# Kernel optimization log

Measured on AMD Instinct MI355X. Metric: run time of the kernel, lower is better.

Reference implementation:

```python
import jax, jax.numpy as jnp
import numpy as np

T, B, A = 64, 512, 5
XD, YD, ZD, HD, MD = 2, 10, 16, 200, 90
HMIC, HMAC = 200, 200


def setup_inputs() -> dict:
    key = jax.random.key(0)
    ks = jax.random.split(key, 40)
    it = iter(range(40))
    def nrm(shape, s=0.05):
        return jax.random.normal(ks[next(it)], shape, jnp.float32) * s
    inp = {}
    inp["y"] = jax.random.normal(ks[next(it)], (T, B, YD), jnp.float32)
    # values in {-1} u [0, MD): -1 means "sample macro goal"
    inp["macro_goals"] = jax.random.randint(ks[next(it)], (T, B, A), 0, MD + 1, jnp.int32) - 1
    # dec_macro: Linear(YD+HMAC,HD) ReLU Linear(HD,MD) LogSoftmax
    inp["Wdm1"] = nrm((A, YD + HMAC, HD)); inp["bdm1"] = nrm((A, HD))
    inp["Wdm2"] = nrm((A, HD, MD));        inp["bdm2"] = nrm((A, MD))
    # prior: Linear(MD+HMIC,HD) ReLU Linear(HD,HD) ReLU
    inp["Wpr1"] = nrm((A, MD + HMIC, HD)); inp["bpr1"] = nrm((A, HD))
    inp["Wpr2"] = nrm((A, HD, HD));        inp["bpr2"] = nrm((A, HD))
    inp["Wpm"] = nrm((A, HD, ZD)); inp["bpm"] = nrm((A, ZD))
    inp["Wps"] = nrm((A, HD, ZD)); inp["bps"] = nrm((A, ZD))
    # dec: Linear(YD+MD+ZD+HMIC,HD) ReLU Linear(HD,HD) ReLU
    inp["Wd1"] = nrm((A, YD + MD + ZD + HMIC, HD)); inp["bd1"] = nrm((A, HD))
    inp["Wd2"] = nrm((A, HD, HD));                  inp["bd2"] = nrm((A, HD))
    inp["Wdx"] = nrm((A, HD, XD)); inp["bdx"] = nrm((A, XD))
    inp["Wds"] = nrm((A, HD, XD)); inp["bds"] = nrm((A, XD))
    # per-agent micro GRU (input XD+ZD, hidden HMIC), torch gate order [r;z;n]
    inp["Wih_mic"] = nrm((A, 3 * HMIC, XD + ZD)); inp["Whh_mic"] = nrm((A, 3 * HMIC, HMIC))
    inp["bih_mic"] = nrm((A, 3 * HMIC));          inp["bhh_mic"] = nrm((A, 3 * HMIC))
    # macro GRU (input A*MD, hidden HMAC)
    inp["Wih_mac"] = nrm((3 * HMAC, A * MD)); inp["Whh_mac"] = nrm((3 * HMAC, HMAC))
    inp["bih_mac"] = nrm((3 * HMAC,));        inp["bhh_mac"] = nrm((3 * HMAC,))
    # pre-drawn sampling noise: gumbel for multinomial, standard normal for gaussians
    u = jax.random.uniform(ks[next(it)], (T - 1, A, B, MD), jnp.float32, 1e-6, 1.0 - 1e-6)
    inp["eps_g"] = -jnp.log(-jnp.log(u))
    inp["eps_z"] = jax.random.normal(ks[next(it)], (T - 1, A, B, ZD), jnp.float32)
    inp["eps_x"] = jax.random.normal(ks[next(it)], (T - 1, A, B, XD), jnp.float32)
    inp["burn_in"] = 8
    return inp


def reference(y, Wdm1, bdm1, Wdm2, bdm2, Wpr1, bpr1, Wpr2, bpr2, Wpm, bpm, Wps, bps,
              Wd1, bd1, Wd2, bd2, Wdx, bdx, Wds, bds,
              Wih_mic, Whh_mic, bih_mic, bhh_mic, Wih_mac, Whh_mac, bih_mac, bhh_mac,
              eps_g, eps_z, eps_x, macro_goals, burn_in):
    def lin(x, W, b):  # per-agent linear: x [A,B,I], W [A,I,O]
        return jnp.einsum('abi,aio->abo', x, W) + b[:, None]

    def gru1(x, h, Wih, Whh, bih, bhh):  # x [B,I], h [B,H]
        gi = x @ Wih.T + bih
        gh = h @ Whh.T + bhh
        ir, iz, inn = jnp.split(gi, 3, -1)
        hr, hz, hn = jnp.split(gh, 3, -1)
        r = jax.nn.sigmoid(ir + hr); zg = jax.nn.sigmoid(iz + hz)
        return (1 - zg) * jnp.tanh(inn + r * hn) + zg * h

    def gruA(x, h, Wih, Whh, bih, bhh):  # x [A,B,I], h [A,B,H]
        gi = jnp.einsum('abi,agi->abg', x, Wih) + bih[:, None]
        gh = jnp.einsum('abh,agh->abg', h, Whh) + bhh[:, None]
        ir, iz, inn = jnp.split(gi, 3, -1)
        hr, hz, hn = jnp.split(gh, 3, -1)
        r = jax.nn.sigmoid(ir + hr); zg = jax.nn.sigmoid(iz + hz)
        return (1 - zg) * jnp.tanh(inn + r * hn) + zg * h

    goals_in = macro_goals[:T - 1, 0, :]  # [T-1, A]; torch code only reads batch row 0

    def step(carry, xs):
        y_t, h_mic, h_mac = carry
        t, curr, g_t, ez_t, ex_t, y_next_true = xs
        yA = jnp.broadcast_to(y_t, (A, B, YD))
        hmacA = jnp.broadcast_to(h_mac, (A, B, HMAC))
        # macro-goal decoder (log-softmax) and goal selection
        hdm = jax.nn.relu(lin(jnp.concatenate([yA, hmacA], -1), Wdm1, bdm1))
        logp = jax.nn.log_softmax(lin(hdm, Wdm2, bdm2), -1)          # [A,B,MD]
        samp_flag = (curr == -1) | ((t >= burn_in) & (burn_in > 0))  # [A]
        sampled = jax.nn.one_hot(jnp.argmax(logp + g_t, -1), MD, dtype=logp.dtype)
        fixed = jnp.zeros((A, B, MD), logp.dtype).at[:, 0, :].set(
            jax.nn.one_hot(curr, MD, dtype=logp.dtype))  # torch sets only batch row 0
        m_t = jnp.where(samp_flag[:, None, None], sampled, fixed)    # [A,B,MD]
        goals_out = jnp.argmax(m_t, -1).T                            # [B,A]
        # macro GRU over concatenated agent goals
        h_mac2 = gru1(jnp.transpose(m_t, (1, 0, 2)).reshape(B, A * MD),
                      h_mac, Wih_mac, Whh_mac, bih_mac, bhh_mac)
        # prior -> sample z
        hp = jax.nn.relu(lin(jax.nn.relu(lin(jnp.concatenate([m_t, h_mic], -1),
                                             Wpr1, bpr1)), Wpr2, bpr2))
        z_t = lin(hp, Wpm, bpm) + jax.nn.softplus(lin(hp, Wps, bps)) * ez_t  # [A,B,ZD]
        # decoder -> sample next positions (teacher-forced during burn-in)
        hd = jax.nn.relu(lin(jax.nn.relu(lin(jnp.concatenate([yA, m_t, z_t, h_mic], -1),
                                             Wd1, bd1)), Wd2, bd2))
        x_samp = lin(hd, Wdx, bdx) + jax.nn.softplus(lin(hd, Wds, bds)) * ex_t  # [A,B,XD]
        x_true = jnp.transpose(y_next_true.reshape(B, A, XD), (1, 0, 2))
        x_next = jnp.where(t < burn_in, x_true, x_samp)
        y_next = jnp.transpose(x_next, (1, 0, 2)).reshape(B, YD)
        # per-agent micro GRUs on [x_next, z]
        h_mic2 = gruA(jnp.concatenate([x_next, z_t], -1), h_mic,
                      Wih_mic, Whh_mic, bih_mic, bhh_mic)
        return (y_next, h_mic2, h_mac2), (y_next, goals_out)

    carry0 = (y[0], jnp.zeros((A, B, HMIC), y.dtype), jnp.zeros((B, HMAC), y.dtype))
    xs = (jnp.arange(T - 1), goals_in, eps_g, eps_z, eps_x, y[1:])
    _, (ys, goals) = jax.lax.scan(step, carry0, xs)
    ret = jnp.concatenate([y[:1], ys], 0)                 # [T,B,YD]
    goals_full = jnp.concatenate([goals, goals[-1:]], 0)  # [T,B,A]; last = second-last
    return ret, goals_full
```

## Files before the change

kernel.cpp:

```cpp
#include <hip/hip_runtime.h>


#define T_STEPS 63
#define BATCH   512
#define NA      5
#define YDIM    10
#define ZDIM    16
#define XDIM    2
#define HD      200
#define MDIM    90
#define HM      200
#define NB      4
#define NT      256
#define NCH     128

struct Params {
  const float *yin;
  const int   *mg;
  const float *Wdm1,*bdm1,*bdm2;
  const float *Wpr1,*bpr1,*Wpr2,*bpr2,*Wpm,*bpm,*Wps,*bps;
  const float *Wd1,*bd1,*Wd2,*bd2,*Wdx,*bdx,*Wds,*bds;
  const float *bih_mic,*bhh_mic,*bih_mac,*bhh_mac;
  const float *eps_g,*eps_z,*eps_x;
  const int   *burn;
  const float *WihTmic,*WhhTmic,*WihTmac,*WhhTmac,*Wdm2p;
  float *hmac_ws,*hmic_ws;
  int   *cidx;
  float *ret,*goals;
};

__device__ __forceinline__ float sigm(float x){ return 1.f/(1.f+expf(-x)); }
__device__ __forceinline__ float softplusf(float x){ return log1pf(expf(-fabsf(x))) + fmaxf(x,0.f); }

template<int NBv>
__device__ __forceinline__ void mv4(const float* __restrict__ W, int N, int K,
                                    const float* __restrict__ act, int astride,
                                    int o, int kseg, float acc[4][NBv])
{
  const int Q = K >> 2;
  const int qpt = (Q + 3) >> 2;
  int q0 = kseg * qpt;
  int q1 = (Q < q0 + qpt) ? Q : (q0 + qpt);
  for (int q = q0; q < q1; ++q) {
    const float* wr = W + (size_t)(4*q)*N + o;
    const float4 w0 = *(const float4*)(wr);
    const float4 w1 = *(const float4*)(wr + N);
    const float4 w2 = *(const float4*)(wr + 2*N);
    const float4 w3 = *(const float4*)(wr + 3*N);
    #pragma unroll
    for (int j = 0; j < NBv; ++j) {
      const float4 av = *(const float4*)(act + j*astride + 4*q);
      acc[0][j] = fmaf(av.x, w0.x, acc[0][j]);
      acc[1][j] = fmaf(av.x, w0.y, acc[1][j]);
      acc[2][j] = fmaf(av.x, w0.z, acc[2][j]);
      acc[3][j] = fmaf(av.x, w0.w, acc[3][j]);
      acc[0][j] = fmaf(av.y, w1.x, acc[0][j]);
      acc[1][j] = fmaf(av.y, w1.y, acc[1][j]);
      acc[2][j] = fmaf(av.y, w1.z, acc[2][j]);
      acc[3][j] = fmaf(av.y, w1.w, acc[3][j]);
      acc[0][j] = fmaf(av.z, w2.x, acc[0][j]);
      acc[1][j] = fmaf(av.z, w2.y, acc[1][j]);
      acc[2][j] = fmaf(av.z, w2.z, acc[2][j]);
      acc[3][j] = fmaf(av.z, w2.w, acc[3][j]);
      acc[0][j] = fmaf(av.w, w3.x, acc[0][j]);
      acc[1][j] = fmaf(av.w, w3.y, acc[1][j]);
      acc[2][j] = fmaf(av.w, w3.z, acc[2][j]);
      acc[3][j] = fmaf(av.w, w3.w, acc[3][j]);
    }
  }
  if (kseg == 3) {
    for (int k = Q*4; k < K; ++k) {
      const float4 w = *(const float4*)(W + (size_t)k*N + o);
      #pragma unroll
      for (int j = 0; j < NBv; ++j) {
        const float a = act[j*astride + k];
        acc[0][j] = fmaf(a, w.x, acc[0][j]);
        acc[1][j] = fmaf(a, w.y, acc[1][j]);
        acc[2][j] = fmaf(a, w.z, acc[2][j]);
        acc[3][j] = fmaf(a, w.w, acc[3][j]);
      }
    }
  }
}

template<int NBv>
__device__ __forceinline__ void qreduce(float acc[4][NBv]) {
  #pragma unroll
  for (int c = 0; c < 4; ++c)
    #pragma unroll
    for (int j = 0; j < NBv; ++j) {
      float v = acc[c][j];
      v += __shfl_xor(v, 1);
      v += __shfl_xor(v, 2);
      acc[c][j] = v;
    }
}

__global__ void prep_kernel(const float* __restrict__ Whh_mac, const float* __restrict__ Whh_mic,
                            const float* __restrict__ Wih_mic, const float* __restrict__ Wih_mac,
                            const float* __restrict__ Wdm2,
                            float* __restrict__ WhhTmac, float* __restrict__ WhhTmic,
                            float* __restrict__ WihTmic, float* __restrict__ WihTmac,
                            float* __restrict__ Wdm2p)
{
  int i = blockIdx.x * 256 + threadIdx.x;
  if (i < 120000) {
    int k = i / 600, g = i % 600;
    WhhTmac[i] = Whh_mac[g*200 + k];
  } else if (i < 720000) {
    int j = i - 120000;
    int a = j / 120000, r = j % 120000;
    int k = r / 600, g = r % 600;
    WhhTmic[j] = Whh_mic[a*120000 + g*200 + k];
  } else if (i < 774000) {
    int j = i - 720000;
    int a = j / 10800, r = j % 10800;
    int k = r / 600, g = r % 600;
    WihTmic[j] = Wih_mic[a*10800 + g*18 + k];
  } else if (i < 1044000) {
    int j = i - 774000;
    int k = j / 600, g = j % 600;
    WihTmac[j] = Wih_mac[g*450 + k];
  } else if (i < 1140000) {
    int j = i - 1044000;
    int a = j / 19200, r = j % 19200;
    int k = r / 96, o = r % 96;
    Wdm2p[j] = (o < 90) ? Wdm2[(a*200 + k)*90 + o] : 0.f;
  }
}

__global__ __launch_bounds__(NT, 4) void step_kernel(Params p, int t)
{
  __shared__ __align__(16) float sHmac[NB][208];
  __shared__ __align__(16) float sHmic[NB][208];
  __shared__ __align__(16) float sXC[NB][20];
  __shared__ __align__(16) float sZ[NB][16];
  __shared__ float sRedM[NB][2][8];
  __shared__ float sRedS[NB][2][8];
  __shared__ __align__(16) union ScratchU {
    float gs[NB][400];
    struct { float b1[NB][208]; float b2[NB][208]; float lg[NB][96]; float y[NB][12]; } m;
  } U;
  __shared__ int sIdxP[NA][NB];
  __shared__ int sMid[NB];

  const int tid = threadIdx.x;
  const int bid = blockIdx.x;
  const int X = bid & 7, slot = bid >> 3;
  const int jj = X * 80 + slot;
  const int a  = jj >> 7;
  const int c  = jj & 127;
  const int b0 = c * NB;
  const int burn = p.burn[0];
  const int og = tid >> 2;
  const int kseg = tid & 3;

  if (t == 0) {
    for (int u = tid; u < NB*HM; u += NT) {
      int j = u / HM, k = u % HM;
      sHmac[j][k] = 0.f; sHmic[j][k] = 0.f;
    }
    if (tid < NB*XDIM) {
      int j = tid >> 1, o = tid & 1;
      p.ret[(b0+j)*YDIM + a*XDIM + o] = p.yin[(b0+j)*YDIM + a*XDIM + o];
    }
  } else {
    for (int u = tid; u < NB*HM; u += NT) {
      int j = u / HM, k = u % HM;
      size_t soff = ((size_t)a*BATCH + b0 + j)*HM + k;
      sHmac[j][k] = p.hmac_ws[soff];
      sHmic[j][k] = p.hmic_ws[soff];
    }
    if (tid < NA*NB) {
      int a2 = tid >> 2, j = tid & 3;
      sIdxP[a2][j] = p.cidx[((t-1)&1)*(NCH*NA*NB) + c*(NA*NB) + a2*NB + j];
    }
  }
  __syncthreads();

  if (t > 0) {
    #pragma unroll 1
    for (int pass = 0; pass < 2; ++pass) {
      int gq = og + pass*64;
      if (gq < 100) {
        int g = gq*4;
        float aI[4][NB], aH[4][NB];
        #pragma unroll
        for (int cc = 0; cc < 4; ++cc)
          #pragma unroll
          for (int j = 0; j < NB; ++j) { aI[cc][j] = 0.f; aH[cc][j] = 0.f; }
        for (int a2 = kseg; a2 < NA; a2 += 4) {
          #pragma unroll
          for (int j = 0; j < NB; ++j) {
            int r = sIdxP[a2][j];
            if (r >= 0) {
              const float4 w = *(const float4*)(p.WihTmac + (size_t)(a2*MDIM + r)*600 + g);
              aI[0][j] += w.x; aI[1][j] += w.y; aI[2][j] += w.z; aI[3][j] += w.w;
            }
          }
        }
        mv4<NB>(p.WhhTmac, 600, HM, &sHmac[0][0], 208, g, kseg, aH);
        qreduce<NB>(aI);
        qreduce<NB>(aH);
        const float4 bi = *(const float4*)(p.bih_mac + g);
        const float4 bh = *(const float4*)(p.bhh_mac + g);
        #pragma unroll
        for (int j = 0; j < NB; ++j) {
          if (j == kseg) {
            *(float4*)&U.gs[j][g] = make_float4(aI[0][j]+bi.x+aH[0][j]+bh.x,
                                                aI[1][j]+bi.y+aH[1][j]+bh.y,
                                                aI[2][j]+bi.z+aH[2][j]+bh.z,
                                                aI[3][j]+bi.w+aH[3][j]+bh.w);
          }
        }
      }
    }
    if (og < 50) {
      int g = 400 + og*4, k4 = og*4;
      float aI[4][NB], aH[4][NB];
      #pragma unroll
      for (int cc = 0; cc < 4; ++cc)
        #pragma unroll
        for (int j = 0; j < NB; ++j) { aI[cc][j] = 0.f; aH[cc][j] = 0.f; }
      for (int a2 = kseg; a2 < NA; a2 += 4) {
        #pragma unroll
        for (int j = 0; j < NB; ++j) {
          int r = sIdxP[a2][j];
          if (r >= 0) {
            const float4 w = *(const float4*)(p.WihTmac + (size_t)(a2*MDIM + r)*600 + g);
            aI[0][j] += w.x; aI[1][j] += w.y; aI[2][j] += w.z; aI[3][j] += w.w;
          }
        }
      }
      mv4<NB>(p.WhhTmac, 600, HM, &sHmac[0][0], 208, g, kseg, aH);
      qreduce<NB>(aI);
      qreduce<NB>(aH);
      const float4 bi = *(const float4*)(p.bih_mac + g);
      const float4 bh = *(const float4*)(p.bhh_mac + g);
      #pragma unroll
      for (int j = 0; j < NB; ++j) {
        if (j == kseg) {
          const float4 r4 = *(const float4*)&U.gs[j][k4];
          *(float4*)&U.gs[j][k4] = make_float4(
            aI[0][j]+bi.x + sigm(r4.x)*(aH[0][j]+bh.x),
            aI[1][j]+bi.y + sigm(r4.y)*(aH[1][j]+bh.y),
            aI[2][j]+bi.z + sigm(r4.z)*(aH[2][j]+bh.z),
            aI[3][j]+bi.w + sigm(r4.w)*(aH[3][j]+bh.w));
        }
      }
    }
    __syncthreads();
    for (int u = tid; u < NB*HM; u += NT) {
      int j = u / HM, k = u % HM;
      float zg = sigm(U.gs[j][200+k]);
      sHmac[j][k] = (1.f - zg)*tanhf(U.gs[j][k]) + zg*sHmac[j][k];
    }
    __syncthreads();
  }

  for (int u = tid; u < NB*YDIM; u += NT) {
    int j = u / YDIM, k = u % YDIM;
    U.m.y[j][k] = (t == 0) ? p.yin[(b0+j)*YDIM + k]
                           : p.ret[(size_t)t*BATCH*YDIM + (b0+j)*YDIM + k];
  }
  __syncthreads();

  if (og < 50) {
    int o = og*4;
    float acc[4][NB];
    #pragma unroll
    for (int cc = 0; cc < 4; ++cc)
      #pragma unroll
      for (int j = 0; j < NB; ++j) acc[cc][j] = 0.f;
    const float* W = p.Wdm1 + (size_t)a*(YDIM+HM)*HD;
    mv4<NB>(W, HD, YDIM, &U.m.y[0][0], 12, o, kseg, acc);
    mv4<NB>(W + (size_t)YDIM*HD, HD, HM, &sHmac[0][0], 208, o, kseg, acc);
    qreduce<NB>(acc);
    const float4 bv = *(const float4*)(p.bdm1 + a*HD + o);
    #pragma unroll
    for (int j = 0; j < NB; ++j) {
      if (j == kseg) {
        *(float4*)&U.m.b1[j][o] = make_float4(
          fmaxf(acc[0][j]+bv.x, 0.f), fmaxf(acc[1][j]+bv.y, 0.f),
          fmaxf(acc[2][j]+bv.z, 0.f), fmaxf(acc[3][j]+bv.w, 0.f));
      }
    }
  }
  __syncthreads();
  if (og < 24) {
    int o = og*4;
    float acc[4][NB];
    #pragma unroll
    for (int cc = 0; cc < 4; ++cc)
      #pragma unroll
      for (int j = 0; j < NB; ++j) acc[cc][j] = 0.f;
    mv4<NB>(p.Wdm2p + (size_t)a*HD*96, 96, HD, &U.m.b1[0][0], 208, o, kseg, acc);
    qreduce<NB>(acc);
    float b0v = (o+0 < MDIM) ? p.bdm2[a*MDIM + o+0] : 0.f;
    float b1v = (o+1 < MDIM) ? p.bdm2[a*MDIM + o+1] : 0.f;
    float b2v = (o+2 < MDIM) ? p.bdm2[a*MDIM + o+2] : 0.f;
    float b3v = (o+3 < MDIM) ? p.bdm2[a*MDIM + o+3] : 0.f;
    #pragma unroll
    for (int j = 0; j < NB; ++j) {
      if (j == kseg) {
        *(float4*)&U.m.lg[j][o] = make_float4(acc[0][j]+b0v, acc[1][j]+b1v,
                                              acc[2][j]+b2v, acc[3][j]+b3v);
      }
    }
  }
  __syncthreads();
  for (int u = tid; u < NB*MDIM; u += NT) {
    int j = u / MDIM, cc = u % MDIM;
    U.m.lg[j][cc] += p.eps_g[(((size_t)t*NA + a)*BATCH + b0 + j)*MDIM + cc];
  }
  __syncthreads();
  if (tid < 32) {
    int j = tid >> 3, s = tid & 7;
    float best = -3.4e38f; int bi2 = 0;
    for (int cc = s; cc < MDIM; cc += 8) {
      float v = U.m.lg[j][cc];
      if (v > best) { best = v; bi2 = cc; }
    }
    #pragma unroll
    for (int d = 1; d < 8; d <<= 1) {
      float ob = __shfl_xor(best, d); int oi = __shfl_xor(bi2, d);
      if (ob > best || (ob == best && oi < bi2)) { best = ob; bi2 = oi; }
    }
    if (s == 0) {
      int curr = p.mg[(size_t)t*BATCH*NA + a];
      bool sf = (curr == -1) || ((t >= burn) && (burn > 0));
      int mi = sf ? bi2 : ((b0 + j) == 0 ? curr : -1);
      sMid[j] = mi;
      float gv = (float)(mi < 0 ? 0 : mi);
      p.goals[(size_t)t*BATCH*NA + (b0+j)*NA + a] = gv;
      if (t == T_STEPS-1) p.goals[(size_t)T_STEPS*BATCH*NA + (b0+j)*NA + a] = gv;
      p.cidx[(t&1)*(NCH*NA*NB) + c*(NA*NB) + a*NB + j] = mi;
    }
  }
  __syncthreads();

  if (og < 50) {
    int o = og*4;
    float acc[4][NB];
    #pragma unroll
    for (int cc = 0; cc < 4; ++cc)
      #pragma unroll
      for (int j = 0; j < NB; ++j) acc[cc][j] = 0.f;
    const float* W = p.Wpr1 + (size_t)a*(MDIM+HM)*HD;
    #pragma unroll
    for (int j = 0; j < NB; ++j) {
      if (j == kseg) {
        int mi = sMid[j];
        if (mi >= 0) {
          const float4 w = *(const float4*)(W + (size_t)mi*HD + o);
          acc[0][j] += w.x; acc[1][j] += w.y; acc[2][j] += w.z; acc[3][j] += w.w;
        }
      }
    }
    mv4<NB>(W + (size_t)MDIM*HD, HD, HM, &sHmic[0][0], 208, o, kseg, acc);
    qreduce<NB>(acc);
    const float4 bv = *(const float4*)(p.bpr1 + a*HD + o);
    #pragma unroll
    for (int j = 0; j < NB; ++j) {
      if (j == kseg) {
        *(float4*)&U.m.b2[j][o] = make_float4(
          fmaxf(acc[0][j]+bv.x, 0.f), fmaxf(acc[1][j]+bv.y, 0.f),
          fmaxf(acc[2][j]+bv.z, 0.f), fmaxf(acc[3][j]+bv.w, 0.f));
      }
    }
  }
  __syncthreads();
  if (og < 50) {
    int o = og*4;
    float acc[4][NB];
    #pragma unroll
    for (int cc = 0; cc < 4; ++cc)
      #pragma unroll
      for (int j = 0; j < NB; ++j) acc[cc][j] = 0.f;
    mv4<NB>(p.Wpr2 + (size_t)a*HD*HD, HD, HD, &U.m.b2[0][0], 208, o, kseg, acc);
    qreduce<NB>(acc);
    const float4 bv = *(const float4*)(p.bpr2 + a*HD + o);
    #pragma unroll
    for (int j = 0; j < NB; ++j) {
      if (j == kseg) {
        *(float4*)&U.m.b1[j][o] = make_float4(
          fmaxf(acc[0][j]+bv.x, 0.f), fmaxf(acc[1][j]+bv.y, 0.f),
          fmaxf(acc[2][j]+bv.z, 0.f), fmaxf(acc[3][j]+bv.w, 0.f));
      }
    }
  }
  __syncthreads();
  {
    int j = tid >> 6, o = (tid >> 2) & 15, s = tid & 3;
    float am = 0.f, as = 0.f;
    const float* wm  = p.Wpm + (size_t)a*HD*ZDIM + o;
    const float* wsp = p.Wps + (size_t)a*HD*ZDIM + o;
    for (int k = s*50; k < s*50 + 50; ++k) {
      float h = U.m.b1[j][k];
      am = fmaf(h, wm[(size_t)k*ZDIM], am);
      as = fmaf(h, wsp[(size_t)k*ZDIM], as);
    }
    am += __shfl_xor(am, 1); am += __shfl_xor(am, 2);
    as += __shfl_xor(as, 1); as += __shfl_xor(as, 2);
    if (s == 0) {
      am += p.bpm[a*ZDIM + o];
      as += p.bps[a*ZDIM + o];
      float zv = am + softplusf(as) * p.eps_z[(((size_t)t*NA + a)*BATCH + b0 + j)*ZDIM + o];
      sZ[j][o] = zv;
      sXC[j][2+o] = zv;
    }
  }
  __syncthreads();

  if (og < 50) {
    int o = og*4;
    float acc[4][NB];
    #pragma unroll
    for (int cc = 0; cc < 4; ++cc)
      #pragma unroll
      for (int j = 0; j < NB; ++j) acc[cc][j] = 0.f;
    const float* W = p.Wd1 + (size_t)a*(YDIM+MDIM+ZDIM+HM)*HD;
    #pragma unroll
    for (int j = 0; j < NB; ++j) {
      if (j == kseg) {
        int mi = sMid[j];
        if (mi >= 0) {
          const float4 w = *(const float4*)(W + (size_t)(YDIM+mi)*HD + o);
          acc[0][j] += w.x; acc[1][j] += w.y; acc[2][j] += w.z; acc[3][j] += w.w;
        }
      }
    }
    mv4<NB>(W, HD, YDIM, &U.m.y[0][0], 12, o, kseg, acc);
    mv4<NB>(W + (size_t)(YDIM+MDIM)*HD, HD, ZDIM, &sZ[0][0], 16, o, kseg, acc);
    mv4<NB>(W + (size_t)(YDIM+MDIM+ZDIM)*HD, HD, HM, &sHmic[0][0], 208, o, kseg, acc);
    qreduce<NB>(acc);
    const float4 bv = *(const float4*)(p.bd1 + a*HD + o);
    #pragma unroll
    for (int j = 0; j < NB; ++j) {
      if (j == kseg) {
        *(float4*)&U.m.b2[j][o] = make_float4(
          fmaxf(acc[0][j]+bv.x, 0.f), fmaxf(acc[1][j]+bv.y, 0.f),
          fmaxf(acc[2][j]+bv.z, 0.f), fmaxf(acc[3][j]+bv.w, 0.f));
      }
    }
  }
  __syncthreads();
  if (og < 50) {
    int o = og*4;
    float acc[4][NB];
    #pragma unroll
    for (int cc = 0; cc < 4; ++cc)
      #pragma unroll
      for (int j = 0; j < NB; ++j) acc[cc][j] = 0.f;
    mv4<NB>(p.Wd2 + (size_t)a*HD*HD, HD, HD, &U.m.b2[0][0], 208, o, kseg, acc);
    qreduce<NB>(acc);
    const float4 bv = *(const float4*)(p.bd2 + a*HD + o);
    #pragma unroll
    for (int j = 0; j < NB; ++j) {
      if (j == kseg) {
        *(float4*)&U.m.b1[j][o] = make_float4(
          fmaxf(acc[0][j]+bv.x, 0.f), fmaxf(acc[1][j]+bv.y, 0.f),
          fmaxf(acc[2][j]+bv.z, 0.f), fmaxf(acc[3][j]+bv.w, 0.f));
      }
    }
  }
  __syncthreads();
  if (tid < 64) {
    int j = tid >> 4, o = (tid >> 3) & 1, seg = tid & 7;
    float am = 0.f, as = 0.f;
    const float* wx  = p.Wdx + (size_t)a*HD*XDIM + o;
    const float* wsd = p.Wds + (size_t)a*HD*XDIM + o;
    for (int k = seg*25; k < seg*25 + 25; ++k) {
      float h = U.m.b1[j][k];
      am = fmaf(h, wx[(size_t)k*XDIM], am);
      as = fmaf(h, wsd[(size_t)k*XDIM], as);
    }
    sRedM[j][o][seg] = am; sRedS[j][o][seg] = as;
  }
  __syncthreads();
  if (tid < NB*XDIM) {
    int j = tid >> 1, o = tid & 1;
    float am = p.bdx[a*XDIM + o], as = p.bds[a*XDIM + o];
    for (int s2 = 0; s2 < 8; ++s2) { am += sRedM[j][o][s2]; as += sRedS[j][o][s2]; }
    float xs = am + softplusf(as) * p.eps_x[(((size_t)t*NA + a)*BATCH + b0 + j)*XDIM + o];
    float xt = p.yin[((size_t)(t+1))*BATCH*YDIM + (b0+j)*YDIM + a*XDIM + o];
    float xv = (t < burn) ? xt : xs;
    p.ret[((size_t)(t+1))*BATCH*YDIM + (b0+j)*YDIM + a*XDIM + o] = xv;
    sXC[j][o] = xv;
  }
  __syncthreads();

  #pragma unroll 1
  for (int pass = 0; pass < 2; ++pass) {
    int gq = og + pass*64;
    if (gq < 100) {
      int g = gq*4;
      float aI[4][NB], aH[4][NB];
      #pragma unroll
      for (int cc = 0; cc < 4; ++cc)
        #pragma unroll
        for (int j = 0; j < NB; ++j) { aI[cc][j] = 0.f; aH[cc][j] = 0.f; }
      mv4<NB>(p.WihTmic + (size_t)a*18*600, 600, 18, &sXC[0][0], 20, g, kseg, aI);
      mv4<NB>(p.WhhTmic + (size_t)a*HM*600, 600, HM, &sHmic[0][0], 208, g, kseg, aH);
      qreduce<NB>(aI);
      qreduce<NB>(aH);
      const float4 bi = *(const float4*)(p.bih_mic + a*600 + g);
      const float4 bh = *(const float4*)(p.bhh_mic + a*600 + g);
      #pragma unroll
      for (int j = 0; j < NB; ++j) {
        if (j == kseg) {
          *(float4*)&U.gs[j][g] = make_float4(aI[0][j]+bi.x+aH[0][j]+bh.x,
                                              aI[1][j]+bi.y+aH[1][j]+bh.y,
                                              aI[2][j]+bi.z+aH[2][j]+bh.z,
                                              aI[3][j]+bi.w+aH[3][j]+bh.w);
        }
      }
    }
  }
  if (og < 50) {
    int g = 400 + og*4, k4 = og*4;
    float aI[4][NB], aH[4][NB];
    #pragma unroll
    for (int cc = 0; cc < 4; ++cc)
      #pragma unroll
      for (int j = 0; j < NB; ++j) { aI[cc][j] = 0.f; aH[cc][j] = 0.f; }
    mv4<NB>(p.WihTmic + (size_t)a*18*600, 600, 18, &sXC[0][0], 20, g, kseg, aI);
    mv4<NB>(p.WhhTmic + (size_t)a*HM*600, 600, HM, &sHmic[0][0], 208, g, kseg, aH);
    qreduce<NB>(aI);
    qreduce<NB>(aH);
    const float4 bi = *(const float4*)(p.bih_mic + a*600 + g);
    const float4 bh = *(const float4*)(p.bhh_mic + a*600 + g);
    #pragma unroll
    for (int j = 0; j < NB; ++j) {
      if (j == kseg) {
        const float4 r4 = *(const float4*)&U.gs[j][k4];
        *(float4*)&U.gs[j][k4] = make_float4(
          aI[0][j]+bi.x + sigm(r4.x)*(aH[0][j]+bh.x),
          aI[1][j]+bi.y + sigm(r4.y)*(aH[1][j]+bh.y),
          aI[2][j]+bi.z + sigm(r4.z)*(aH[2][j]+bh.z),
          aI[3][j]+bi.w + sigm(r4.w)*(aH[3][j]+bh.w));
      }
    }
  }
  __syncthreads();
  for (int u = tid; u < NB*HM; u += NT) {
    int j = u / HM, k = u % HM;
    float zg = sigm(U.gs[j][200+k]);
    float nh = (1.f - zg)*tanhf(U.gs[j][k]) + zg*sHmic[j][k];
    size_t soff = ((size_t)a*BATCH + b0 + j)*HM + k;
    p.hmic_ws[soff] = nh;
    p.hmac_ws[soff] = sHmac[j][k];
  }
}

extern "C" void kernel_launch(void* const* d_in, const int* in_sizes, int n_in,
                              void* d_out, int out_size, void* d_ws, size_t ws_size,
                              hipStream_t stream) {
  (void)in_sizes; (void)n_in; (void)out_size; (void)ws_size;
  Params p;
  p.yin   = (const float*)d_in[0];
  p.mg    = (const int*)  d_in[1];
  p.Wdm1  = (const float*)d_in[2];  p.bdm1 = (const float*)d_in[3];
  const float* Wdm2 = (const float*)d_in[4];
  p.bdm2  = (const float*)d_in[5];
  p.Wpr1  = (const float*)d_in[6];  p.bpr1 = (const float*)d_in[7];
  p.Wpr2  = (const float*)d_in[8];  p.bpr2 = (const float*)d_in[9];
  p.Wpm   = (const float*)d_in[10]; p.bpm  = (const float*)d_in[11];
  p.Wps   = (const float*)d_in[12]; p.bps  = (const float*)d_in[13];
  p.Wd1   = (const float*)d_in[14]; p.bd1  = (const float*)d_in[15];
  p.Wd2   = (const float*)d_in[16]; p.bd2  = (const float*)d_in[17];
  p.Wdx   = (const float*)d_in[18]; p.bdx  = (const float*)d_in[19];
  p.Wds   = (const float*)d_in[20]; p.bds  = (const float*)d_in[21];
  const float* Wih_mic = (const float*)d_in[22];
  const float* Whh_mic = (const float*)d_in[23];
  p.bih_mic = (const float*)d_in[24]; p.bhh_mic = (const float*)d_in[25];
  const float* Wih_mac = (const float*)d_in[26];
  const float* Whh_mac = (const float*)d_in[27];
  p.bih_mac = (const float*)d_in[28]; p.bhh_mac = (const float*)d_in[29];
  p.eps_g = (const float*)d_in[30];
  p.eps_z = (const float*)d_in[31];
  p.eps_x = (const float*)d_in[32];
  p.burn  = (const int*)  d_in[33];

  float* ws = (float*)d_ws;
  float* WhhTmac = ws;
  float* WhhTmic = ws + 120000;
  float* WihTmic = ws + 720000;
  float* WihTmac = ws + 774000;
  float* Wdm2p   = ws + 1044000;
  p.hmac_ws = ws + 1140000;
  p.hmic_ws = ws + 1652000;
  p.cidx = (int*)(ws + 2164000);
  p.WhhTmac = WhhTmac; p.WhhTmic = WhhTmic; p.WihTmic = WihTmic; p.WihTmac = WihTmac;
  p.Wdm2p = Wdm2p;

  p.ret   = (float*)d_out;
  p.goals = (float*)d_out + (size_t)(T_STEPS+1)*BATCH*YDIM;

  prep_kernel<<<(1140000 + 255)/256, 256, 0, stream>>>(
      Whh_mac, Whh_mic, Wih_mic, Wih_mac, Wdm2,
      WhhTmac, WhhTmic, WihTmic, WihTmac, Wdm2p);

  for (int t = 0; t < T_STEPS; ++t)
    step_kernel<<<NA*NCH, NT, 0, stream>>>(p, t);
}
```

Baseline: 11.66 ms.

## Split macro GRU into separate kernel to stop redundant per-agent recomputation

The macro GRU update was computed redundantly by all five agent blocks of each batch chunk. It now runs once per chunk in a new mac_kernel launched before each step kernel, and its hidden state is stored once per batch instead of once per agent. The matvec inner loop also gains register double-buffering of weight loads, and the noise tensors are read with nontemporal loads. In exchange, each time step now needs an extra kernel launch, and the macro kernel runs on only 128 blocks.

```diff
diff --git a/kernel.cpp b/kernel.cpp
--- a/kernel.cpp
+++ b/kernel.cpp
@@ -24,7 +24,8 @@
   const float *eps_g,*eps_z,*eps_x;
   const int   *burn;
   const float *WihTmic,*WhhTmic,*WihTmac,*WhhTmac,*Wdm2p;
-  float *hmac_ws,*hmic_ws;
+  float *hmac_ws;
+  float *hmic_ws;
   int   *cidx;
   float *ret,*goals;
 };
@@ -39,33 +40,44 @@
 {
   const int Q = K >> 2;
   const int qpt = (Q + 3) >> 2;
-  int q0 = kseg * qpt;
-  int q1 = (Q < q0 + qpt) ? Q : (q0 + qpt);
-  for (int q = q0; q < q1; ++q) {
-    const float* wr = W + (size_t)(4*q)*N + o;
-    const float4 w0 = *(const float4*)(wr);
-    const float4 w1 = *(const float4*)(wr + N);
-    const float4 w2 = *(const float4*)(wr + 2*N);
-    const float4 w3 = *(const float4*)(wr + 3*N);
-    #pragma unroll
-    for (int j = 0; j < NBv; ++j) {
-      const float4 av = *(const float4*)(act + j*astride + 4*q);
-      acc[0][j] = fmaf(av.x, w0.x, acc[0][j]);
-      acc[1][j] = fmaf(av.x, w0.y, acc[1][j]);
-      acc[2][j] = fmaf(av.x, w0.z, acc[2][j]);
-      acc[3][j] = fmaf(av.x, w0.w, acc[3][j]);
-      acc[0][j] = fmaf(av.y, w1.x, acc[0][j]);
-      acc[1][j] = fmaf(av.y, w1.y, acc[1][j]);
-      acc[2][j] = fmaf(av.y, w1.z, acc[2][j]);
-      acc[3][j] = fmaf(av.y, w1.w, acc[3][j]);
-      acc[0][j] = fmaf(av.z, w2.x, acc[0][j]);
-      acc[1][j] = fmaf(av.z, w2.y, acc[1][j]);
-      acc[2][j] = fmaf(av.z, w2.z, acc[2][j]);
-      acc[3][j] = fmaf(av.z, w2.w, acc[3][j]);
-      acc[0][j] = fmaf(av.w, w3.x, acc[0][j]);
-      acc[1][j] = fmaf(av.w, w3.y, acc[1][j]);
-      acc[2][j] = fmaf(av.w, w3.z, acc[2][j]);
-      acc[3][j] = fmaf(av.w, w3.w, acc[3][j]);
+  const int q0 = kseg * qpt;
+  const int q1 = (Q < q0 + qpt) ? Q : (q0 + qpt);
+  if (q0 < q1) {
+    const float* wr = W + (size_t)(4*q0)*N + o;
+    float4 w0 = *(const float4*)(wr);
+    float4 w1 = *(const float4*)(wr + N);
+    float4 w2 = *(const float4*)(wr + 2*N);
+    float4 w3 = *(const float4*)(wr + 3*N);
+    for (int q = q0; q < q1; ++q) {
+      float4 n0 = w0, n1 = w1, n2 = w2, n3 = w3;
+      const float* wn = wr + (size_t)4*N;
+      if (q + 1 < q1) {
+        n0 = *(const float4*)(wn);
+        n1 = *(const float4*)(wn + N);
+        n2 = *(const float4*)(wn + 2*N);
+        n3 = *(const float4*)(wn + 3*N);
+      }
+      #pragma unroll
+      for (int j = 0; j < NBv; ++j) {
+        const float4 av = *(const float4*)(act + j*astride + 4*q);
+        acc[0][j] = fmaf(av.x, w0.x, acc[0][j]);
+        acc[1][j] = fmaf(av.x, w0.y, acc[1][j]);
+        acc[2][j] = fmaf(av.x, w0.z, acc[2][j]);
+        acc[3][j] = fmaf(av.x, w0.w, acc[3][j]);
+        acc[0][j] = fmaf(av.y, w1.x, acc[0][j]);
+        acc[1][j] = fmaf(av.y, w1.y, acc[1][j]);
+        acc[2][j] = fmaf(av.y, w1.z, acc[2][j]);
+        acc[3][j] = fmaf(av.y, w1.w, acc[3][j]);
+        acc[0][j] = fmaf(av.z, w2.x, acc[0][j]);
+        acc[1][j] = fmaf(av.z, w2.y, acc[1][j]);
+        acc[2][j] = fmaf(av.z, w2.z, acc[2][j]);
+        acc[3][j] = fmaf(av.z, w2.w, acc[3][j]);
+        acc[0][j] = fmaf(av.w, w3.x, acc[0][j]);
+        acc[1][j] = fmaf(av.w, w3.y, acc[1][j]);
+        acc[2][j] = fmaf(av.w, w3.z, acc[2][j]);
+        acc[3][j] = fmaf(av.w, w3.w, acc[3][j]);
+      }
+      w0 = n0; w1 = n1; w2 = n2; w3 = n3; wr = wn;
     }
   }
   if (kseg == 3) {
@@ -129,6 +141,106 @@
   }
 }
 
+__global__ __launch_bounds__(NT, 4) void mac_kernel(Params p, int t)
+{
+  __shared__ __align__(16) float sH[NB][208];
+  __shared__ __align__(16) float gs[NB][400];
+  __shared__ int sIdx[NA][NB];
+
+  const int tid = threadIdx.x;
+  const int c = blockIdx.x;
+  const int b0 = c * NB;
+  const int og = tid >> 2;
+  const int kseg = tid & 3;
+
+  for (int u = tid; u < NB*HM; u += NT) {
+    int j = u / HM, k = u % HM;
+    sH[j][k] = (t == 1) ? 0.f : p.hmac_ws[(size_t)(b0 + j)*HM + k];
+  }
+  if (tid < NA*NB) {
+    int a2 = tid >> 2, j = tid & 3;
+    sIdx[a2][j] = p.cidx[((t-1)&1)*(NCH*NA*NB) + c*(NA*NB) + a2*NB + j];
+  }
+  __syncthreads();
+
+  #pragma unroll 1
+  for (int pass = 0; pass < 2; ++pass) {
+    int gq = og + pass*64;
+    if (gq < 100) {
+      int g = gq*4;
+      float aI[4][NB], aH[4][NB];
+      #pragma unroll
+      for (int cc = 0; cc < 4; ++cc)
+        #pragma unroll
+        for (int j = 0; j < NB; ++j) { aI[cc][j] = 0.f; aH[cc][j] = 0.f; }
+      for (int a2 = kseg; a2 < NA; a2 += 4) {
+        #pragma unroll
+        for (int j = 0; j < NB; ++j) {
+          int r = sIdx[a2][j];
+          if (r >= 0) {
+            const float4 w = *(const float4*)(p.WihTmac + (size_t)(a2*MDIM + r)*600 + g);
+            aI[0][j] += w.x; aI[1][j] += w.y; aI[2][j] += w.z; aI[3][j] += w.w;
+          }
+        }
+      }
+      mv4<NB>(p.WhhTmac, 600, HM, &sH[0][0], 208, g, kseg, aH);
+      qreduce<NB>(aI);
+      qreduce<NB>(aH);
+      const float4 bi = *(const float4*)(p.bih_mac + g);
+      const float4 bh = *(const float4*)(p.bhh_mac + g);
+      #pragma unroll
+      for (int j = 0; j < NB; ++j) {
+        if (j == kseg) {
+          *(float4*)&gs[j][g] = make_float4(aI[0][j]+bi.x+aH[0][j]+bh.x,
+                                            aI[1][j]+bi.y+aH[1][j]+bh.y,
+                                            aI[2][j]+bi.z+aH[2][j]+bh.z,
+                                            aI[3][j]+bi.w+aH[3][j]+bh.w);
+        }
+      }
+    }
+  }
+  if (og < 50) {
+    int g = 400 + og*4, k4 = og*4;
+    float aI[4][NB], aH[4][NB];
+    #pragma unroll
+    for (int cc = 0; cc < 4; ++cc)
+      #pragma unroll
+      for (int j = 0; j < NB; ++j) { aI[cc][j] = 0.f; aH[cc][j] = 0.f; }
+    for (int a2 = kseg; a2 < NA; a2 += 4) {
+      #pragma unroll
+      for (int j = 0; j < NB; ++j) {
+        int r = sIdx[a2][j];
+        if (r >= 0) {
+          const float4 w = *(const float4*)(p.WihTmac + (size_t)(a2*MDIM + r)*600 + g);
+          aI[0][j] += w.x; aI[1][j] += w.y; aI[2][j] += w.z; aI[3][j] += w.w;
+        }
+      }
+    }
+    mv4<NB>(p.WhhTmac, 600, HM, &sH[0][0], 208, g, kseg, aH);
+    qreduce<NB>(aI);
+    qreduce<NB>(aH);
+    const float4 bi = *(const float4*)(p.bih_mac + g);
+    const float4 bh = *(const float4*)(p.bhh_mac + g);
+    #pragma unroll
+    for (int j = 0; j < NB; ++j) {
+      if (j == kseg) {
+        const float4 r4 = *(const float4*)&gs[j][k4];
+        *(float4*)&gs[j][k4] = make_float4(
+          aI[0][j]+bi.x + sigm(r4.x)*(aH[0][j]+bh.x),
+          aI[1][j]+bi.y + sigm(r4.y)*(aH[1][j]+bh.y),
+          aI[2][j]+bi.z + sigm(r4.z)*(aH[2][j]+bh.z),
+          aI[3][j]+bi.w + sigm(r4.w)*(aH[3][j]+bh.w));
+      }
+    }
+  }
+  __syncthreads();
+  for (int u = tid; u < NB*HM; u += NT) {
+    int j = u / HM, k = u % HM;
+    float zg = sigm(gs[j][200+k]);
+    p.hmac_ws[(size_t)(b0+j)*HM + k] = (1.f - zg)*tanhf(gs[j][k]) + zg*sH[j][k];
+  }
+}
+
 __global__ __launch_bounds__(NT, 4) void step_kernel(Params p, int t)
 {
   __shared__ __align__(16) float sHmac[NB][208];
@@ -141,7 +253,6 @@
     float gs[NB][400];
     struct { float b1[NB][208]; float b2[NB][208]; float lg[NB][96]; float y[NB][12]; } m;
   } U;
-  __shared__ int sIdxP[NA][NB];
   __shared__ int sMid[NB];
 
   const int tid = threadIdx.x;
@@ -167,96 +278,11 @@
   } else {
     for (int u = tid; u < NB*HM; u += NT) {
       int j = u / HM, k = u % HM;
-      size_t soff = ((size_t)a*BATCH + b0 + j)*HM + k;
-      sHmac[j][k] = p.hmac_ws[soff];
-      sHmic[j][k] = p.hmic_ws[soff];
-    }
-    if (tid < NA*NB) {
-      int a2 = tid >> 2, j = tid & 3;
-      sIdxP[a2][j] = p.cidx[((t-1)&1)*(NCH*NA*NB) + c*(NA*NB) + a2*NB + j];
-    }
-  }
-  __syncthreads();
-
-  if (t > 0) {
-    #pragma unroll 1
-    for (int pass = 0; pass < 2; ++pass) {
-      int gq = og + pass*64;
-      if (gq < 100) {
-        int g = gq*4;
-        float aI[4][NB], aH[4][NB];
-        #pragma unroll
-        for (int cc = 0; cc < 4; ++cc)
-          #pragma unroll
-          for (int j = 0; j < NB; ++j) { aI[cc][j] = 0.f; aH[cc][j] = 0.f; }
-        for (int a2 = kseg; a2 < NA; a2 += 4) {
-          #pragma unroll
-          for (int j = 0; j < NB; ++j) {
-            int r = sIdxP[a2][j];
-            if (r >= 0) {
-              const float4 w = *(const float4*)(p.WihTmac + (size_t)(a2*MDIM + r)*600 + g);
-              aI[0][j] += w.x; aI[1][j] += w.y; aI[2][j] += w.z; aI[3][j] += w.w;
-            }
-          }
-        }
-        mv4<NB>(p.WhhTmac, 600, HM, &sHmac[0][0], 208, g, kseg, aH);
-        qreduce<NB>(aI);
-        qreduce<NB>(aH);
-        const float4 bi = *(const float4*)(p.bih_mac + g);
-        const float4 bh = *(const float4*)(p.bhh_mac + g);
-        #pragma unroll
-        for (int j = 0; j < NB; ++j) {
-          if (j == kseg) {
-            *(float4*)&U.gs[j][g] = make_float4(aI[0][j]+bi.x+aH[0][j]+bh.x,
-                                                aI[1][j]+bi.y+aH[1][j]+bh.y,
-                                                aI[2][j]+bi.z+aH[2][j]+bh.z,
-                                                aI[3][j]+bi.w+aH[3][j]+bh.w);
-          }
-        }
-      }
-    }
-    if (og < 50) {
-      int g = 400 + og*4, k4 = og*4;
-      float aI[4][NB], aH[4][NB];
-      #pragma unroll
-      for (int cc = 0; cc < 4; ++cc)
-        #pragma unroll
-        for (int j = 0; j < NB; ++j) { aI[cc][j] = 0.f; aH[cc][j] = 0.f; }
-      for (int a2 = kseg; a2 < NA; a2 += 4) {
-        #pragma unroll
-        for (int j = 0; j < NB; ++j) {
-          int r = sIdxP[a2][j];
-          if (r >= 0) {
-            const float4 w = *(const float4*)(p.WihTmac + (size_t)(a2*MDIM + r)*600 + g);
-            aI[0][j] += w.x; aI[1][j] += w.y; aI[2][j] += w.z; aI[3][j] += w.w;
-          }
-        }
-      }
-      mv4<NB>(p.WhhTmac, 600, HM, &sHmac[0][0], 208, g, kseg, aH);
-      qreduce<NB>(aI);
-      qreduce<NB>(aH);
-      const float4 bi = *(const float4*)(p.bih_mac + g);
-      const float4 bh = *(const float4*)(p.bhh_mac + g);
-      #pragma unroll
-      for (int j = 0; j < NB; ++j) {
-        if (j == kseg) {
-          const float4 r4 = *(const float4*)&U.gs[j][k4];
-          *(float4*)&U.gs[j][k4] = make_float4(
-            aI[0][j]+bi.x + sigm(r4.x)*(aH[0][j]+bh.x),
-            aI[1][j]+bi.y + sigm(r4.y)*(aH[1][j]+bh.y),
-            aI[2][j]+bi.z + sigm(r4.z)*(aH[2][j]+bh.z),
-            aI[3][j]+bi.w + sigm(r4.w)*(aH[3][j]+bh.w));
-        }
-      }
-    }
-    __syncthreads();
-    for (int u = tid; u < NB*HM; u += NT) {
-      int j = u / HM, k = u % HM;
-      float zg = sigm(U.gs[j][200+k]);
-      sHmac[j][k] = (1.f - zg)*tanhf(U.gs[j][k]) + zg*sHmac[j][k];
-    }
-    __syncthreads();
-  }
+      sHmac[j][k] = p.hmac_ws[(size_t)(b0 + j)*HM + k];
+      sHmic[j][k] = p.hmic_ws[((size_t)a*BATCH + b0 + j)*HM + k];
+    }
+  }
+  __syncthreads();
 
   for (int u = tid; u < NB*YDIM; u += NT) {
     int j = u / YDIM, k = u % YDIM;
@@ -311,7 +337,8 @@
   __syncthreads();
   for (int u = tid; u < NB*MDIM; u += NT) {
     int j = u / MDIM, cc = u % MDIM;
-    U.m.lg[j][cc] += p.eps_g[(((size_t)t*NA + a)*BATCH + b0 + j)*MDIM + cc];
+    U.m.lg[j][cc] += __builtin_nontemporal_load(
+        &p.eps_g[(((size_t)t*NA + a)*BATCH + b0 + j)*MDIM + cc]);
   }
   __syncthreads();
   if (tid < 32) {
@@ -349,7 +376,7 @@
     const float* W = p.Wpr1 + (size_t)a*(MDIM+HM)*HD;
     #pragma unroll
     for (int j = 0; j < NB; ++j) {
-      if (j == kseg) {
+      if (kseg == j) {
         int mi = sMid[j];
         if (mi >= 0) {
           const float4 w = *(const float4*)(W + (size_t)mi*HD + o);
@@ -405,7 +432,8 @@
     if (s == 0) {
       am += p.bpm[a*ZDIM + o];
       as += p.bps[a*ZDIM + o];
-      float zv = am + softplusf(as) * p.eps_z[(((size_t)t*NA + a)*BATCH + b0 + j)*ZDIM + o];
+      float zv = am + softplusf(as) * __builtin_nontemporal_load(
+          &p.eps_z[(((size_t)t*NA + a)*BATCH + b0 + j)*ZDIM + o]);
       sZ[j][o] = zv;
       sXC[j][2+o] = zv;
     }
@@ -422,7 +450,7 @@
     const float* W = p.Wd1 + (size_t)a*(YDIM+MDIM+ZDIM+HM)*HD;
     #pragma unroll
     for (int j = 0; j < NB; ++j) {
-      if (j == kseg) {
+      if (kseg == j) {
         int mi = sMid[j];
         if (mi >= 0) {
           const float4 w = *(const float4*)(W + (size_t)(YDIM+mi)*HD + o);
@@ -482,7 +510,8 @@
     int j = tid >> 1, o = tid & 1;
     float am = p.bdx[a*XDIM + o], as = p.bds[a*XDIM + o];
     for (int s2 = 0; s2 < 8; ++s2) { am += sRedM[j][o][s2]; as += sRedS[j][o][s2]; }
-    float xs = am + softplusf(as) * p.eps_x[(((size_t)t*NA + a)*BATCH + b0 + j)*XDIM + o];
+    float xs = am + softplusf(as) * __builtin_nontemporal_load(
+        &p.eps_x[(((size_t)t*NA + a)*BATCH + b0 + j)*XDIM + o]);
     float xt = p.yin[((size_t)(t+1))*BATCH*YDIM + (b0+j)*YDIM + a*XDIM + o];
     float xv = (t < burn) ? xt : xs;
     p.ret[((size_t)(t+1))*BATCH*YDIM + (b0+j)*YDIM + a*XDIM + o] = xv;
@@ -547,9 +576,7 @@
     int j = u / HM, k = u % HM;
     float zg = sigm(U.gs[j][200+k]);
     float nh = (1.f - zg)*tanhf(U.gs[j][k]) + zg*sHmic[j][k];
-    size_t soff = ((size_t)a*BATCH + b0 + j)*HM + k;
-    p.hmic_ws[soff] = nh;
-    p.hmac_ws[soff] = sHmac[j][k];
+    p.hmic_ws[((size_t)a*BATCH + b0 + j)*HM + k] = nh;
   }
 }
 
@@ -589,8 +616,8 @@
   float* WihTmac = ws + 774000;
   float* Wdm2p   = ws + 1044000;
   p.hmac_ws = ws + 1140000;
-  p.hmic_ws = ws + 1652000;
-  p.cidx = (int*)(ws + 2164000);
+  p.hmic_ws = ws + 1242400;
+  p.cidx = (int*)(ws + 1754400);
   p.WhhTmac = WhhTmac; p.WhhTmic = WhhTmic; p.WihTmic = WihTmic; p.WihTmac = WihTmac;
   p.Wdm2p = Wdm2p;
 
@@ -601,6 +628,8 @@
       Whh_mac, Whh_mic, Wih_mic, Wih_mac, Wdm2,
       WhhTmac, WhhTmic, WihTmic, WihTmac, Wdm2p);
 
-  for (int t = 0; t < T_STEPS; ++t)
+  for (int t = 0; t < T_STEPS; ++t) {
+    if (t > 0) mac_kernel<<<NCH, NT, 0, stream>>>(p, t);
     step_kernel<<<NA*NCH, NT, 0, stream>>>(p, t);
+  }
 }
```

Measured after the change: 10.80 ms. 7.4% less time.
